# Kernel optimization log

Measured on AMD Instinct MI355X. Metric: run time of the kernel, lower is better.

Reference implementation:

```python
import jax, jax.numpy as jnp
import numpy as np

H = 8      # num_attention_heads
DH = 96    # attention_head_size
LN_EPS = 1e-5


def setup_inputs() -> dict:
    key = jax.random.key(0)
    ks = jax.random.split(key, 12)
    B, S, D = 2, 768, 768
    sc = 0.02
    return {
        "hidden_states": jax.random.normal(ks[0], (B, S, D), jnp.float32),
        "distance_matrix": jax.random.uniform(ks[1], (B, S, S), jnp.float32) * 20.0,
        "angle_matrix": jax.random.uniform(ks[2], (B, S, S), jnp.float32) * np.pi,
        "attention_mask": jnp.ones((B, S), jnp.float32),
        "Wq": jax.random.normal(ks[3], (D, D), jnp.float32) * sc,
        "bq": jnp.zeros((D,), jnp.float32),
        "Wk": jax.random.normal(ks[4], (D, D), jnp.float32) * sc,
        "bk": jnp.zeros((D,), jnp.float32),
        "Wv": jax.random.normal(ks[5], (D, D), jnp.float32) * sc,
        "bv": jnp.zeros((D,), jnp.float32),
        "Wd": jax.random.normal(ks[6], (DH,), jnp.float32) * sc,
        "bd": jnp.zeros((DH,), jnp.float32),
        "Wa": jax.random.normal(ks[7], (DH,), jnp.float32) * sc,
        "ba": jnp.zeros((DH,), jnp.float32),
        "Wo": jax.random.normal(ks[8], (D, D), jnp.float32) * sc,
        "bo": jnp.zeros((D,), jnp.float32),
        "ln_g": jnp.ones((D,), jnp.float32),
        "ln_b": jnp.zeros((D,), jnp.float32),
    }


def _heads(x, B, S):
    # [B,S,D] -> [B,H,S,DH]
    return x.reshape(B, S, H, DH).transpose(0, 2, 1, 3)


def reference(hidden_states, distance_matrix, angle_matrix, attention_mask,
              Wq, bq, Wk, bk, Wv, bv, Wd, bd, Wa, ba, Wo, bo, ln_g, ln_b):
    B, S, D = hidden_states.shape
    q = _heads(hidden_states @ Wq.T + bq, B, S)   # [B,H,S,DH]
    k = _heads(hidden_states @ Wk.T + bk, B, S)
    v = _heads(hidden_states @ Wv.T + bv, B, S)

    scores = jnp.einsum('bhid,bhjd->bhij', q, k) / jnp.sqrt(jnp.float32(DH))

    # distance / angle relative-position biases: emb[b,i,j,:] = dist[b,i,j]*Wd + bd
    dist_emb = distance_matrix[..., None] * Wd + bd   # [B,S,S,DH]
    scores = scores + jnp.einsum('bhid,bijd->bhij', q, dist_emb)
    ang_emb = angle_matrix[..., None] * Wa + ba       # [B,S,S,DH]
    scores = scores + jnp.einsum('bhid,bijd->bhij', q, ang_emb)

    # key mask, broadcast over heads and query positions
    scores = scores + (1.0 - attention_mask)[:, None, None, :] * -10000.0

    probs = jax.nn.softmax(scores, axis=-1)           # [B,H,S,S]
    ctx = jnp.einsum('bhij,bhjd->bhid', probs, v)
    ctx = ctx.transpose(0, 2, 1, 3).reshape(B, S, D)  # [B,S,D]

    out = ctx @ Wo.T + bo
    x = out + hidden_states
    mu = jnp.mean(x, axis=-1, keepdims=True)
    var = jnp.var(x, axis=-1, keepdims=True)
    out = (x - mu) * jax.lax.rsqrt(var + LN_EPS) * ln_g + ln_b
    return out, probs
```

## Files before the change

kernel.cpp:

```cpp
#include <hip/hip_runtime.h>
#include <stdint.h>

#define B_  2
#define S_  768
#define D_  768
#define H_  8
#define DH_ 96

typedef unsigned short ushort_t;
typedef __bf16 bf16x8 __attribute__((ext_vector_type(8)));
typedef float  f32x4  __attribute__((ext_vector_type(4)));
typedef _Float16 f16x4 __attribute__((ext_vector_type(4)));

__device__ inline ushort_t f2bf(float f) {
    union { float f; unsigned int u; } v; v.f = f;
    unsigned int u = v.u;
    unsigned int r = u + 0x7fffu + ((u >> 16) & 1u);
    return (ushort_t)(r >> 16);
}
__device__ inline float bf2f(ushort_t u) {
    union { unsigned int i; float f; } c; c.i = ((unsigned int)u) << 16;
    return c.f;
}
__device__ inline ushort_t f2h(float f) {
    union { _Float16 h; ushort_t u; } c; c.h = (_Float16)f; return c.u;
}

__device__ inline void glds16(const void* gp, void* lp) {
    auto g = reinterpret_cast<const __attribute__((address_space(1))) uint32_t*>(
        reinterpret_cast<uintptr_t>(gp));
    auto l = reinterpret_cast<__attribute__((address_space(3))) uint32_t*>(
        reinterpret_cast<uintptr_t>(lp));
    __builtin_amdgcn_global_load_lds(g, l, 16, 0, 0);
}

__global__ __launch_bounds__(256) void k_convert(
        const float* __restrict__ X, const float* __restrict__ Wq,
        const float* __restrict__ Wk, const float* __restrict__ Wv,
        const float* __restrict__ Wo, const float* __restrict__ distm,
        const float* __restrict__ angm,
        ushort_t* __restrict__ Xb, ushort_t* __restrict__ Wb,
        ushort_t* __restrict__ Dh, ushort_t* __restrict__ Ah) {
    const int NX4 = (B_ * S_ * D_) / 4;
    const int NW4 = (D_ * D_) / 4;
    const int NWall = 4 * NW4;
    const int ND4 = (B_ * S_ * S_) / 4;
    int i = blockIdx.x * blockDim.x + threadIdx.x;
    float4 v;
    ushort_t* dst;
    bool h16 = false;
    if (i < NX4) {
        v = ((const float4*)X)[i];
        dst = Xb + i * 4;
    } else if (i < NX4 + NWall) {
        int wi = i - NX4;
        int sel = wi / NW4;
        int off = wi - sel * NW4;
        const float* src = (sel == 0) ? Wq : (sel == 1) ? Wk : (sel == 2) ? Wv : Wo;
        v = ((const float4*)src)[off];
        dst = Wb + wi * 4;
    } else if (i < NX4 + NWall + ND4) {
        int off = i - NX4 - NWall;
        v = ((const float4*)distm)[off];
        dst = Dh + off * 4; h16 = true;
    } else {
        int off = i - NX4 - NWall - ND4;
        v = ((const float4*)angm)[off];
        dst = Ah + off * 4; h16 = true;
    }
    ushort4 o;
    if (h16) { o.x = f2h(v.x); o.y = f2h(v.y); o.z = f2h(v.z); o.w = f2h(v.w); }
    else     { o.x = f2bf(v.x); o.y = f2bf(v.y); o.z = f2bf(v.z); o.w = f2bf(v.w); }
    *(ushort4*)dst = o;
}

__device__ inline void gemm64_dbuf(
        const ushort_t* __restrict__ A, int lda,
        const ushort_t* __restrict__ Bt, int ldb,
        int K, int m0, int n0,
        ushort_t* As, ushort_t* Bs, f32x4 acc[2][2]) {
    const int tid  = threadIdx.x;
    const int lane = tid & 63, wave = tid >> 6;
    const int wm = (wave >> 1) * 32, wn = (wave & 1) * 32;
    const int fr = lane & 15, fk = (lane >> 4) * 8;
    const ushort_t* Ap = A  + (size_t)(m0 + wave * 16 + (lane >> 2)) * lda + (lane & 3) * 8;
    const ushort_t* Bp = Bt + (size_t)(n0 + wave * 16 + (lane >> 2)) * ldb + (lane & 3) * 8;
    glds16(Ap, As + wave * 512);
    glds16(Bp, Bs + wave * 512);
    for (int kt = 0; kt < K; kt += 32) {
        const int cur = (kt >> 5) & 1;
        __syncthreads();
        if (kt + 32 < K) {
            glds16(Ap + kt + 32, As + (cur ^ 1) * 2048 + wave * 512);
            glds16(Bp + kt + 32, Bs + (cur ^ 1) * 2048 + wave * 512);
        }
        const ushort_t* Ab = As + cur * 2048;
        const ushort_t* Bb = Bs + cur * 2048;
        bf16x8 a0 = *(const bf16x8*)&Ab[(wm      + fr) * 32 + fk];
        bf16x8 a1 = *(const bf16x8*)&Ab[(wm + 16 + fr) * 32 + fk];
        bf16x8 b0 = *(const bf16x8*)&Bb[(wn      + fr) * 32 + fk];
        bf16x8 b1 = *(const bf16x8*)&Bb[(wn + 16 + fr) * 32 + fk];
        acc[0][0] = __builtin_amdgcn_mfma_f32_16x16x32_bf16(a0, b0, acc[0][0], 0, 0, 0);
        acc[0][1] = __builtin_amdgcn_mfma_f32_16x16x32_bf16(a0, b1, acc[0][1], 0, 0, 0);
        acc[1][0] = __builtin_amdgcn_mfma_f32_16x16x32_bf16(a1, b0, acc[1][0], 0, 0, 0);
        acc[1][1] = __builtin_amdgcn_mfma_f32_16x16x32_bf16(a1, b1, acc[1][1], 0, 0, 0);
    }
}

__global__ __launch_bounds__(256) void k_qkv(
        const ushort_t* __restrict__ Xb, const ushort_t* __restrict__ Wb,
        const float* __restrict__ bq, const float* __restrict__ bk,
        const float* __restrict__ bv,
        ushort_t* __restrict__ Qb, ushort_t* __restrict__ Kb,
        ushort_t* __restrict__ Vtb) {
    __shared__ __align__(16) ushort_t As[2][128 * 32];
    __shared__ __align__(16) ushort_t Bs[2][128 * 32];
    const int tid = threadIdx.x, lane = tid & 63, w = tid >> 6;
    const int m0 = blockIdx.y * 128, n0 = blockIdx.x * 128;
    const int frn = lane & 15, fko = (lane >> 4) * 8, frg4 = (lane >> 4) * 4;
    const int wm = (w >> 1) * 64, wn = (w & 1) * 64;
    const int srow = lane >> 2, scol = (lane & 3) * 8;
    f32x4 acc[4][4];
    #pragma unroll
    for (int i = 0; i < 4; i++)
        #pragma unroll
        for (int j = 0; j < 4; j++) acc[i][j] = (f32x4){0.f, 0.f, 0.f, 0.f};
    auto stageAB = [&](int kt, int buf) {
        #pragma unroll
        for (int t = 0; t < 2; ++t) {
            int ins = w * 2 + t;
            int row = ins * 16 + srow;
            glds16(Xb + (size_t)(m0 + row) * D_ + kt + scol, &As[buf][ins * 512]);
            glds16(Wb + (size_t)(n0 + row) * D_ + kt + scol, &Bs[buf][ins * 512]);
        }
    };
    stageAB(0, 0);
    for (int kt = 0; kt < D_; kt += 32) {
        const int cur = (kt >> 5) & 1;
        __syncthreads();
        if (kt + 32 < D_) stageAB(kt + 32, cur ^ 1);
        bf16x8 af[4], bfr[4];
        #pragma unroll
        for (int i = 0; i < 4; ++i) {
            af[i]  = *(const bf16x8*)&As[cur][(wm + i * 16 + frn) * 32 + fko];
            bfr[i] = *(const bf16x8*)&Bs[cur][(wn + i * 16 + frn) * 32 + fko];
        }
        #pragma unroll
        for (int i = 0; i < 4; ++i)
            #pragma unroll
            for (int j = 0; j < 4; ++j)
                acc[i][j] = __builtin_amdgcn_mfma_f32_16x16x32_bf16(af[i], bfr[j], acc[i][j], 0, 0, 0);
    }
    #pragma unroll
    for (int j = 0; j < 4; ++j) {
        int gcol = n0 + wn + j * 16 + frn;
        int gsel = gcol / D_, d768 = gcol - gsel * D_;
        int h = d768 / DH_, d = d768 - h * DH_;
        float bias = (gsel == 0 ? bq : (gsel == 1 ? bk : bv))[d768];
        #pragma unroll
        for (int i = 0; i < 4; ++i) {
            int grow0 = m0 + wm + i * 16 + frg4;
            int b = grow0 / S_, s0 = grow0 - b * S_;
            int bh = b * H_ + h;
            if (gsel == 2) {
                ushort4 o4;
                o4.x = f2bf(acc[i][j][0] + bias);
                o4.y = f2bf(acc[i][j][1] + bias);
                o4.z = f2bf(acc[i][j][2] + bias);
                o4.w = f2bf(acc[i][j][3] + bias);
                *(ushort4*)&Vtb[((size_t)bh * DH_ + d) * S_ + s0] = o4;
            } else if (gsel == 1) {
                #pragma unroll
                for (int r = 0; r < 4; r++)
                    Kb[(((size_t)bh * 12 + (d >> 3)) * S_ + s0 + r) * 8 + (d & 7)] =
                        f2bf(acc[i][j][r] + bias);
            } else {
                #pragma unroll
                for (int r = 0; r < 4; r++)
                    Qb[((size_t)bh * S_ + s0 + r) * DH_ + d] = f2bf(acc[i][j][r] + bias);
            }
        }
    }
}

__global__ __launch_bounds__(256) void k_qcoef(
        const ushort_t* __restrict__ Qb,
        const float* __restrict__ Wd, const float* __restrict__ bd,
        const float* __restrict__ Wa, const float* __restrict__ ba,
        float* __restrict__ qcoef) {
    const int wave = threadIdx.x >> 6, lane = threadIdx.x & 63;
    const int row = blockIdx.x * 4 + wave;
    const ushort_t* q = Qb + (size_t)row * DH_;
    float e0 = bf2f(q[lane]);
    float c0 = e0 * Wd[lane];
    float c1 = e0 * Wa[lane];
    float c2 = e0 * (bd[lane] + ba[lane]);
    if (lane < 32) {
        int d = 64 + lane;
        float e1 = bf2f(q[d]);
        c0 += e1 * Wd[d];
        c1 += e1 * Wa[d];
        c2 += e1 * (bd[d] + ba[d]);
    }
    #pragma unroll
    for (int o = 32; o > 0; o >>= 1) {
        c0 += __shfl_down(c0, o);
        c1 += __shfl_down(c1, o);
        c2 += __shfl_down(c2, o);
    }
    if (lane == 0) {
        qcoef[row * 3 + 0] = c0;
        qcoef[row * 3 + 1] = c1;
        qcoef[row * 3 + 2] = c2;
    }
}

#define FL1B 16384
#define VBUF 24576
__global__ __launch_bounds__(256, 3) void k_flash(
        const ushort_t* __restrict__ Qb, const ushort_t* __restrict__ Kb,
        const ushort_t* __restrict__ Vtb, const float* __restrict__ qcoef,
        const ushort_t* __restrict__ Dh, const ushort_t* __restrict__ Ah,
        const float* __restrict__ mask,
        float* __restrict__ probs, ushort_t* __restrict__ Ctxb) {
    __shared__ __align__(16) char sm[2 * VBUF + 512];
    float* mstat = (float*)(sm + 2 * VBUF);
    float* lstat = (float*)(sm + 2 * VBUF + 256);
    const int idx = blockIdx.x;
    const int bh = idx & 15, t = idx >> 4;
    const int b = bh >> 3, h = bh & 7;
    const int r0 = t * 16;
    const int tid = threadIdx.x, lane = tid & 63, w = tid >> 6;
    const int frn = lane & 15, g = lane >> 4;
    const ushort_t* Qbh = Qb + (size_t)bh * S_ * DH_;
    const ushort_t* Kbh = Kb + (size_t)bh * 12 * S_ * 8;
    const ushort_t* Vbh = Vtb + (size_t)bh * DH_ * S_;

    auto stage = [&](int c) {
        char* bufc = sm + (c & 1) * FL1B;
        ushort_t* Ks = (ushort_t*)bufc;
        #pragma unroll
        for (int tt = 0; tt < 3; ++tt) {
            int grp = w * 3 + tt;
            glds16(Kbh + (((size_t)grp * S_ + c * 64 + lane) << 3), Ks + grp * 512);
        }
        int row8 = ((w & 1) << 3) + (lane >> 3);
        int usrc = (2 * (lane & 7)) ^ (row8 & 14);
        const ushort_t* srcm = (w >> 1) ? Ah : Dh;
        glds16(srcm + ((size_t)(b * S_ + r0 + row8)) * S_ + c * 64 + usrc * 4,
               bufc + 12288 + ((w >> 1) << 11) + ((w & 1) << 10));
    };
    auto stage_v = [&](int p) {
        ushort_t* Vs = (ushort_t*)(sm + (p & 1) * VBUF);
        const int c0 = p * 128;
        #pragma unroll
        for (int tt = 0; tt < 6; ++tt) {
            int q = w * 6 + tt;
            int d = 4 * q + (lane >> 4);
            int ug = (lane & 15) ^ (d & 15);
            glds16(Vbh + (size_t)d * S_ + c0 + ug * 8, Vs + q * 512);
        }
    };

    stage(0);

    bf16x8 aq0, aq1, aq2;
    {
        const ushort_t* qp = Qbh + (size_t)(r0 + frn) * DH_ + g * 8;
        aq0 = *(const bf16x8*)qp;
        aq1 = *(const bf16x8*)(qp + 32);
        aq2 = *(const bf16x8*)(qp + 64);
    }
    float qc0, qc1, qc2;
    {
        const float* qp = qcoef + ((size_t)bh * S_ + r0 + frn) * 3;
        qc0 = qp[0]; qc1 = qp[1]; qc2 = qp[2];
    }
    const float isq = 0.10206207261596577f;
    const int daswz = (((w * 4 + g) ^ (frn & 14)) << 2);
    const int jrow = (16 * w + frn) * 8;

    f32x4 acc[12];
    __syncthreads();
    #pragma unroll
    for (int c = 0; c < 12; ++c) {
        if (c < 11) stage(c + 1);
        char* bufc = sm + (c & 1) * FL1B;
        const ushort_t* Ks = (const ushort_t*)bufc;
        bf16x8 k0 = *(const bf16x8*)&Ks[(g    ) * 512 + jrow];
        bf16x8 k1 = *(const bf16x8*)&Ks[(g + 4) * 512 + jrow];
        bf16x8 k2 = *(const bf16x8*)&Ks[(g + 8) * 512 + jrow];
        f32x4 ca = (f32x4){0.f, 0.f, 0.f, 0.f};
        ca = __builtin_amdgcn_mfma_f32_16x16x32_bf16(k0, aq0, ca, 0, 0, 0);
        ca = __builtin_amdgcn_mfma_f32_16x16x32_bf16(k1, aq1, ca, 0, 0, 0);
        ca = __builtin_amdgcn_mfma_f32_16x16x32_bf16(k2, aq2, ca, 0, 0, 0);
        f16x4 d4 = *(const f16x4*)((const ushort_t*)(bufc + 12288) + frn * 64 + daswz);
        f16x4 a4 = *(const f16x4*)((const ushort_t*)(bufc + 14336) + frn * 64 + daswz);
        float4 m4 = *(const float4*)(mask + b * S_ + c * 64 + w * 16 + g * 4);
        f32x4 o;
        o[0] = ca[0] * isq + (float)d4[0] * qc0 + (float)a4[0] * qc1 + qc2 + (1.f - m4.x) * -10000.f;
        o[1] = ca[1] * isq + (float)d4[1] * qc0 + (float)a4[1] * qc1 + qc2 + (1.f - m4.y) * -10000.f;
        o[2] = ca[2] * isq + (float)d4[2] * qc0 + (float)a4[2] * qc1 + qc2 + (1.f - m4.z) * -10000.f;
        o[3] = ca[3] * isq + (float)d4[3] * qc0 + (float)a4[3] * qc1 + qc2 + (1.f - m4.w) * -10000.f;
        acc[c] = o;
        __syncthreads();
    }

    stage_v(0);
    float mx = -1e30f;
    #pragma unroll
    for (int c = 0; c < 12; ++c)
        #pragma unroll
        for (int r = 0; r < 4; ++r) mx = fmaxf(mx, acc[c][r]);
    mx = fmaxf(mx, __shfl_xor(mx, 16));
    mx = fmaxf(mx, __shfl_xor(mx, 32));
    if (g == 0) mstat[w * 16 + frn] = mx;
    __syncthreads();
    float mf = fmaxf(fmaxf(mstat[frn], mstat[16 + frn]),
                     fmaxf(mstat[32 + frn], mstat[48 + frn]));
    float sum = 0.f;
    #pragma unroll
    for (int c = 0; c < 12; ++c)
        #pragma unroll
        for (int r = 0; r < 4; ++r) {
            float e = __expf(acc[c][r] - mf);
            acc[c][r] = e;
            sum += e;
        }
    sum += __shfl_xor(sum, 16);
    sum += __shfl_xor(sum, 32);
    if (g == 0) lstat[w * 16 + frn] = sum;
    __syncthreads();
    float inv = 1.f / (lstat[frn] + lstat[16 + frn] + lstat[32 + frn] + lstat[48 + frn]);

    f32x4 accO[6];
    #pragma unroll
    for (int i = 0; i < 6; ++i) accO[i] = (f32x4){0.f, 0.f, 0.f, 0.f};
    float* prow = probs + ((size_t)bh * S_ + r0 + frn) * S_ + w * 16 + g * 4;
    const int vsub = (g & 1) << 2;
    const int u0 = 2 * w + (g >> 1);
    #pragma unroll
    for (int p = 0; p < 6; ++p) {
        if (p < 5) stage_v(p + 1);
        const ushort_t* Vs = (const ushort_t*)(sm + (p & 1) * VBUF);
        const int c = 2 * p;
        float4 pw;
        pw.x = acc[c][0] * inv; pw.y = acc[c][1] * inv;
        pw.z = acc[c][2] * inv; pw.w = acc[c][3] * inv;
        *(float4*)(prow + c * 64) = pw;
        pw.x = acc[c + 1][0] * inv; pw.y = acc[c + 1][1] * inv;
        pw.z = acc[c + 1][2] * inv; pw.w = acc[c + 1][3] * inv;
        *(float4*)(prow + (c + 1) * 64) = pw;
        union { bf16x8 v; ushort_t u[8]; } pa;
        #pragma unroll
        for (int r = 0; r < 4; ++r) {
            pa.u[r]     = f2bf(acc[c][r]);
            pa.u[r + 4] = f2bf(acc[c + 1][r]);
        }
        #pragma unroll
        for (int nt = 0; nt < 6; ++nt) {
            int d = nt * 16 + frn;
            const ushort_t* vr = Vs + d * 128 + vsub;
            union { bf16x8 v; uint2 q2[2]; } vb;
            vb.q2[0] = *(const uint2*)(vr + (((u0    ) ^ frn) << 3));
            vb.q2[1] = *(const uint2*)(vr + (((u0 + 8) ^ frn) << 3));
            accO[nt] = __builtin_amdgcn_mfma_f32_16x16x32_bf16(pa.v, vb.v, accO[nt], 0, 0, 0);
        }
        __syncthreads();
    }

    float* ctxred = (float*)sm;
    {
        int zr = tid >> 4, zc = tid & 15;
        #pragma unroll
        for (int i = 0; i < 6; ++i) ctxred[zr * 100 + i * 16 + zc] = 0.f;
    }
    __syncthreads();
    #pragma unroll
    for (int nt = 0; nt < 6; ++nt)
        #pragma unroll
        for (int r = 0; r < 4; ++r)
            atomicAdd(&ctxred[(4 * g + r) * 100 + nt * 16 + frn], accO[nt][r]);
    __syncthreads();
    {
        int zr = tid >> 4, zc = tid & 15;
        float ivr = 1.f / (lstat[zr] + lstat[16 + zr] + lstat[32 + zr] + lstat[48 + zr]);
        ushort_t* crow = Ctxb + ((size_t)b * S_ + r0 + zr) * D_ + h * DH_;
        #pragma unroll
        for (int i = 0; i < 6; ++i)
            crow[i * 16 + zc] = f2bf(ctxred[zr * 100 + i * 16 + zc] * ivr);
    }
}

__global__ __launch_bounds__(256) void k_out(
        const ushort_t* __restrict__ Ctxb, const ushort_t* __restrict__ Wob,
        const float* __restrict__ bo, const float* __restrict__ hidden,
        float* __restrict__ xbuf) {
    __shared__ __align__(16) ushort_t As[2 * 64 * 32];
    __shared__ __align__(16) ushort_t Bs[2 * 64 * 32];
    f32x4 acc[2][2];
    #pragma unroll
    for (int i = 0; i < 2; i++)
        #pragma unroll
        for (int j = 0; j < 2; j++) acc[i][j] = (f32x4){0.f, 0.f, 0.f, 0.f};
    const int m0 = blockIdx.y * 64, n0 = blockIdx.x * 64;
    gemm64_dbuf(Ctxb, D_, Wob, D_, D_, m0, n0, As, Bs, acc);
    const int lane = threadIdx.x & 63, wave = threadIdx.x >> 6;
    const int wm = (wave >> 1) * 32, wn = (wave & 1) * 32;
    #pragma unroll
    for (int ni = 0; ni < 2; ni++) {
        int gcol = n0 + wn + ni * 16 + (lane & 15);
        float bias = bo[gcol];
        #pragma unroll
        for (int mi = 0; mi < 2; mi++) {
            #pragma unroll
            for (int r = 0; r < 4; r++) {
                int grow = m0 + wm + mi * 16 + (lane >> 4) * 4 + r;
                xbuf[(size_t)grow * D_ + gcol] =
                    acc[mi][ni][r] + bias + hidden[(size_t)grow * D_ + gcol];
            }
        }
    }
}

__global__ __launch_bounds__(256) void k_ln(
        const float* __restrict__ xbuf, const float* __restrict__ g,
        const float* __restrict__ bb, float* __restrict__ out) {
    const float* x = xbuf + (size_t)blockIdx.x * D_;
    const int t = threadIdx.x;
    float a0 = x[t], a1 = x[t + 256], a2 = x[t + 512];
    float s = a0 + a1 + a2;
    float ss = a0 * a0 + a1 * a1 + a2 * a2;
    __shared__ float r1[4], r2[4];
    #pragma unroll
    for (int o = 32; o > 0; o >>= 1) { s += __shfl_down(s, o); ss += __shfl_down(ss, o); }
    if ((t & 63) == 0) { r1[t >> 6] = s; r2[t >> 6] = ss; }
    __syncthreads();
    float ts = r1[0] + r1[1] + r1[2] + r1[3];
    float tss = r2[0] + r2[1] + r2[2] + r2[3];
    float mu = ts * (1.0f / D_);
    float var = tss * (1.0f / D_) - mu * mu;
    float rstd = rsqrtf(var + 1e-5f);
    float* o = out + (size_t)blockIdx.x * D_;
    o[t]       = (a0 - mu) * rstd * g[t]       + bb[t];
    o[t + 256] = (a1 - mu) * rstd * g[t + 256] + bb[t + 256];
    o[t + 512] = (a2 - mu) * rstd * g[t + 512] + bb[t + 512];
}

extern "C" void kernel_launch(void* const* d_in, const int* in_sizes, int n_in,
                              void* d_out, int out_size, void* d_ws, size_t ws_size,
                              hipStream_t stream) {
    const float* X     = (const float*)d_in[0];
    const float* distm = (const float*)d_in[1];
    const float* angm  = (const float*)d_in[2];
    const float* mask  = (const float*)d_in[3];
    const float* Wq    = (const float*)d_in[4];
    const float* bq    = (const float*)d_in[5];
    const float* Wk    = (const float*)d_in[6];
    const float* bk    = (const float*)d_in[7];
    const float* Wv    = (const float*)d_in[8];
    const float* bv    = (const float*)d_in[9];
    const float* Wd    = (const float*)d_in[10];
    const float* bd    = (const float*)d_in[11];
    const float* Wa    = (const float*)d_in[12];
    const float* ba    = (const float*)d_in[13];
    const float* Wo    = (const float*)d_in[14];
    const float* bo    = (const float*)d_in[15];
    const float* ln_g  = (const float*)d_in[16];
    const float* ln_b  = (const float*)d_in[17];

    float* outp  = (float*)d_out;
    float* probs = (float*)d_out + (size_t)B_ * S_ * D_;

    char* ws = (char*)d_ws;
    ushort_t* Xb    = (ushort_t*)(ws + 0);
    ushort_t* Wb    = (ushort_t*)(ws + 2359296);
    ushort_t* Qb    = (ushort_t*)(ws + 7077888);
    ushort_t* Kb    = (ushort_t*)(ws + 9437184);
    ushort_t* Vtb   = (ushort_t*)(ws + 11796480);
    ushort_t* Ctxb  = (ushort_t*)(ws + 14155776);
    float*    qcoef = (float*)   (ws + 16515072);
    float*    xbuf  = (float*)   (ws + 16662528);
    ushort_t* Dh    = (ushort_t*)(ws + 16662528);
    ushort_t* Ah    = (ushort_t*)(ws + 16662528 + 2359296);

    k_convert<<<5760, 256, 0, stream>>>(X, Wq, Wk, Wv, Wo, distm, angm, Xb, Wb, Dh, Ah);
    k_qkv<<<dim3(18, 12), 256, 0, stream>>>(Xb, Wb, bq, bk, bv, Qb, Kb, Vtb);
    k_qcoef<<<3072, 256, 0, stream>>>(Qb, Wd, bd, Wa, ba, qcoef);
    k_flash<<<768, 256, 0, stream>>>(Qb, Kb, Vtb, qcoef, Dh, Ah, mask, probs, Ctxb);
    k_out<<<dim3(12, 24), 256, 0, stream>>>(Ctxb, Wb + (size_t)2304 * 768, bo, X, xbuf);
    k_ln<<<1536, 256, 0, stream>>>(xbuf, ln_g, ln_b, outp);
}
```

Before: 191.7 us.

## Replace syncthreads with explicit waitcnt barriers and fuse qcoef into flash kernel

Swaps __syncthreads in the GEMM, QKV and flash loops for raw s_barrier plus explicit vmcnt/lgkmcnt waits under sched_barrier fences. Outstanding async global-to-LDS loads can then stay in flight across the barrier instead of being fully drained. Separately, the per-row q·Wd/q·Wa/q·(bd+ba) coefficients are now computed inside the flash kernel from the Q fragments it already holds, which removes the k_qcoef launch and its global round trip. The hand-counted vmcnt values are fragile: a wrong count would cause LDS races, and the sched barriers limit how the compiler can interleave instructions.

```diff
diff --git a/kernel.cpp b/kernel.cpp
--- a/kernel.cpp
+++ b/kernel.cpp
@@ -33,6 +33,13 @@
         reinterpret_cast<uintptr_t>(lp));
     __builtin_amdgcn_global_load_lds(g, l, 16, 0, 0);
 }
+
+#define SBAR()  { __builtin_amdgcn_sched_barrier(0); __builtin_amdgcn_s_barrier(); \
+                  __builtin_amdgcn_sched_barrier(0); }
+#define WAIT_VM(N) { asm volatile("s_waitcnt vmcnt(" #N ")" ::: "memory"); \
+                     __builtin_amdgcn_sched_barrier(0); }
+#define WAIT_LGKM0() { asm volatile("s_waitcnt lgkmcnt(0)" ::: "memory"); \
+                       __builtin_amdgcn_sched_barrier(0); }
 
 __global__ __launch_bounds__(256) void k_convert(
         const float* __restrict__ X, const float* __restrict__ Wq,
@@ -89,11 +96,14 @@
     glds16(Bp, Bs + wave * 512);
     for (int kt = 0; kt < K; kt += 32) {
         const int cur = (kt >> 5) & 1;
-        __syncthreads();
         if (kt + 32 < K) {
             glds16(Ap + kt + 32, As + (cur ^ 1) * 2048 + wave * 512);
             glds16(Bp + kt + 32, Bs + (cur ^ 1) * 2048 + wave * 512);
-        }
+            WAIT_VM(2)
+        } else {
+            WAIT_VM(0)
+        }
+        SBAR()
         const ushort_t* Ab = As + cur * 2048;
         const ushort_t* Bb = Bs + cur * 2048;
         bf16x8 a0 = *(const bf16x8*)&Ab[(wm      + fr) * 32 + fk];
@@ -104,6 +114,8 @@
         acc[0][1] = __builtin_amdgcn_mfma_f32_16x16x32_bf16(a0, b1, acc[0][1], 0, 0, 0);
         acc[1][0] = __builtin_amdgcn_mfma_f32_16x16x32_bf16(a1, b0, acc[1][0], 0, 0, 0);
         acc[1][1] = __builtin_amdgcn_mfma_f32_16x16x32_bf16(a1, b1, acc[1][1], 0, 0, 0);
+        WAIT_LGKM0()
+        SBAR()
     }
 }
 
@@ -137,8 +149,13 @@
     stageAB(0, 0);
     for (int kt = 0; kt < D_; kt += 32) {
         const int cur = (kt >> 5) & 1;
-        __syncthreads();
-        if (kt + 32 < D_) stageAB(kt + 32, cur ^ 1);
+        if (kt + 32 < D_) {
+            stageAB(kt + 32, cur ^ 1);
+            WAIT_VM(4)
+        } else {
+            WAIT_VM(0)
+        }
+        SBAR()
         bf16x8 af[4], bfr[4];
         #pragma unroll
         for (int i = 0; i < 4; ++i) {
@@ -150,6 +167,8 @@
             #pragma unroll
             for (int j = 0; j < 4; ++j)
                 acc[i][j] = __builtin_amdgcn_mfma_f32_16x16x32_bf16(af[i], bfr[j], acc[i][j], 0, 0, 0);
+        WAIT_LGKM0()
+        SBAR()
     }
     #pragma unroll
     for (int j = 0; j < 4; ++j) {
@@ -183,43 +202,13 @@
     }
 }
 
-__global__ __launch_bounds__(256) void k_qcoef(
-        const ushort_t* __restrict__ Qb,
-        const float* __restrict__ Wd, const float* __restrict__ bd,
-        const float* __restrict__ Wa, const float* __restrict__ ba,
-        float* __restrict__ qcoef) {
-    const int wave = threadIdx.x >> 6, lane = threadIdx.x & 63;
-    const int row = blockIdx.x * 4 + wave;
-    const ushort_t* q = Qb + (size_t)row * DH_;
-    float e0 = bf2f(q[lane]);
-    float c0 = e0 * Wd[lane];
-    float c1 = e0 * Wa[lane];
-    float c2 = e0 * (bd[lane] + ba[lane]);
-    if (lane < 32) {
-        int d = 64 + lane;
-        float e1 = bf2f(q[d]);
-        c0 += e1 * Wd[d];
-        c1 += e1 * Wa[d];
-        c2 += e1 * (bd[d] + ba[d]);
-    }
-    #pragma unroll
-    for (int o = 32; o > 0; o >>= 1) {
-        c0 += __shfl_down(c0, o);
-        c1 += __shfl_down(c1, o);
-        c2 += __shfl_down(c2, o);
-    }
-    if (lane == 0) {
-        qcoef[row * 3 + 0] = c0;
-        qcoef[row * 3 + 1] = c1;
-        qcoef[row * 3 + 2] = c2;
-    }
-}
-
 #define FL1B 16384
 #define VBUF 24576
 __global__ __launch_bounds__(256, 3) void k_flash(
         const ushort_t* __restrict__ Qb, const ushort_t* __restrict__ Kb,
-        const ushort_t* __restrict__ Vtb, const float* __restrict__ qcoef,
+        const ushort_t* __restrict__ Vtb,
+        const float* __restrict__ Wd, const float* __restrict__ bd,
+        const float* __restrict__ Wa, const float* __restrict__ ba,
         const ushort_t* __restrict__ Dh, const ushort_t* __restrict__ Ah,
         const float* __restrict__ mask,
         float* __restrict__ probs, ushort_t* __restrict__ Ctxb) {
@@ -271,20 +260,37 @@
         aq1 = *(const bf16x8*)(qp + 32);
         aq2 = *(const bf16x8*)(qp + 64);
     }
-    float qc0, qc1, qc2;
-    {
-        const float* qp = qcoef + ((size_t)bh * S_ + r0 + frn) * 3;
-        qc0 = qp[0]; qc1 = qp[1]; qc2 = qp[2];
-    }
+    float qc0 = 0.f, qc1 = 0.f, qc2 = 0.f;
+    #pragma unroll
+    for (int f = 0; f < 3; ++f) {
+        bf16x8 aq = (f == 0) ? aq0 : (f == 1) ? aq1 : aq2;
+        #pragma unroll
+        for (int e = 0; e < 8; ++e) {
+            int d = f * 32 + g * 8 + e;
+            float qv = (float)aq[e];
+            qc0 += qv * Wd[d];
+            qc1 += qv * Wa[d];
+            qc2 += qv * (bd[d] + ba[d]);
+        }
+    }
+    qc0 += __shfl_xor(qc0, 16); qc0 += __shfl_xor(qc0, 32);
+    qc1 += __shfl_xor(qc1, 16); qc1 += __shfl_xor(qc1, 32);
+    qc2 += __shfl_xor(qc2, 16); qc2 += __shfl_xor(qc2, 32);
+
     const float isq = 0.10206207261596577f;
     const int daswz = (((w * 4 + g) ^ (frn & 14)) << 2);
     const int jrow = (16 * w + frn) * 8;
 
     f32x4 acc[12];
-    __syncthreads();
     #pragma unroll
     for (int c = 0; c < 12; ++c) {
-        if (c < 11) stage(c + 1);
+        if (c < 11) {
+            stage(c + 1);
+            WAIT_VM(4)
+        } else {
+            WAIT_VM(0)
+        }
+        SBAR()
         char* bufc = sm + (c & 1) * FL1B;
         const ushort_t* Ks = (const ushort_t*)bufc;
         bf16x8 k0 = *(const bf16x8*)&Ks[(g    ) * 512 + jrow];
@@ -303,7 +309,8 @@
         o[2] = ca[2] * isq + (float)d4[2] * qc0 + (float)a4[2] * qc1 + qc2 + (1.f - m4.z) * -10000.f;
         o[3] = ca[3] * isq + (float)d4[3] * qc0 + (float)a4[3] * qc1 + qc2 + (1.f - m4.w) * -10000.f;
         acc[c] = o;
-        __syncthreads();
+        WAIT_LGKM0()
+        SBAR()
     }
 
     stage_v(0);
@@ -315,7 +322,8 @@
     mx = fmaxf(mx, __shfl_xor(mx, 16));
     mx = fmaxf(mx, __shfl_xor(mx, 32));
     if (g == 0) mstat[w * 16 + frn] = mx;
-    __syncthreads();
+    WAIT_LGKM0()
+    SBAR()
     float mf = fmaxf(fmaxf(mstat[frn], mstat[16 + frn]),
                      fmaxf(mstat[32 + frn], mstat[48 + frn]));
     float sum = 0.f;
@@ -330,7 +338,8 @@
     sum += __shfl_xor(sum, 16);
     sum += __shfl_xor(sum, 32);
     if (g == 0) lstat[w * 16 + frn] = sum;
-    __syncthreads();
+    WAIT_LGKM0()
+    SBAR()
     float inv = 1.f / (lstat[frn] + lstat[16 + frn] + lstat[32 + frn] + lstat[48 + frn]);
 
     f32x4 accO[6];
@@ -341,7 +350,11 @@
     const int u0 = 2 * w + (g >> 1);
     #pragma unroll
     for (int p = 0; p < 6; ++p) {
-        if (p < 5) stage_v(p + 1);
+        if (p < 5) { stage_v(p + 1); __builtin_amdgcn_sched_barrier(0); }
+        if (p == 0)     { WAIT_VM(6) }
+        else if (p < 5) { WAIT_VM(8) }
+        else            { WAIT_VM(2) }
+        SBAR()
         const ushort_t* Vs = (const ushort_t*)(sm + (p & 1) * VBUF);
         const int c = 2 * p;
         float4 pw;
@@ -366,7 +379,8 @@
             vb.q2[1] = *(const uint2*)(vr + (((u0 + 8) ^ frn) << 3));
             accO[nt] = __builtin_amdgcn_mfma_f32_16x16x32_bf16(pa.v, vb.v, accO[nt], 0, 0, 0);
         }
-        __syncthreads();
+        WAIT_LGKM0()
+        SBAR()
     }
 
     float* ctxred = (float*)sm;
@@ -479,15 +493,13 @@
     ushort_t* Kb    = (ushort_t*)(ws + 9437184);
     ushort_t* Vtb   = (ushort_t*)(ws + 11796480);
     ushort_t* Ctxb  = (ushort_t*)(ws + 14155776);
-    float*    qcoef = (float*)   (ws + 16515072);
     float*    xbuf  = (float*)   (ws + 16662528);
     ushort_t* Dh    = (ushort_t*)(ws + 16662528);
     ushort_t* Ah    = (ushort_t*)(ws + 16662528 + 2359296);
 
     k_convert<<<5760, 256, 0, stream>>>(X, Wq, Wk, Wv, Wo, distm, angm, Xb, Wb, Dh, Ah);
     k_qkv<<<dim3(18, 12), 256, 0, stream>>>(Xb, Wb, bq, bk, bv, Qb, Kb, Vtb);
-    k_qcoef<<<3072, 256, 0, stream>>>(Qb, Wd, bd, Wa, ba, qcoef);
-    k_flash<<<768, 256, 0, stream>>>(Qb, Kb, Vtb, qcoef, Dh, Ah, mask, probs, Ctxb);
+    k_flash<<<768, 256, 0, stream>>>(Qb, Kb, Vtb, Wd, bd, Wa, ba, Dh, Ah, mask, probs, Ctxb);
     k_out<<<dim3(12, 24), 256, 0, stream>>>(Ctxb, Wb + (size_t)2304 * 768, bo, X, xbuf);
     k_ln<<<1536, 256, 0, stream>>>(xbuf, ln_g, ln_b, outp);
 }
```

Result: faster. 186.2 us (-2.9%).
